# Kernel optimization log

Hardware: AMD Instinct MI355X
Metric: run time of the kernel (lower is better)

The kernel has to match this reference:

```python
import jax, jax.numpy as jnp
import numpy as np

B_, L_, D_, R_, N_ = 8, 1024, 512, 32, 16  # batch, seq(in_channels), dim(=dim_inner), dt_rank, d_state


def setup_inputs() -> dict:
    key = jax.random.key(0)
    ks = jax.random.split(key, 8)
    s = lambda k, shape, scale: jax.random.normal(k, shape, dtype=jnp.float32) * scale
    inv = D_ ** -0.5
    return {
        "x": jax.random.uniform(ks[0], (B_, L_, D_), dtype=jnp.float32),
        "W1": s(ks[1], (D_, D_), inv), "b1": jnp.zeros((D_,), jnp.float32),
        "W2": s(ks[2], (D_, D_), inv), "b2": jnp.zeros((D_,), jnp.float32),
        "Wout": s(ks[3], (D_, D_), inv), "bout": jnp.zeros((D_,), jnp.float32),
        "conv_w": s(ks[4], (L_, L_, 3), (3 * L_) ** -0.5),  # Conv1d(L_, L_, k=3) weight (O,I,W)
        "conv_b": jnp.zeros((L_,), jnp.float32),
        "W_dbc": s(ks[5], (R_ + 2 * N_, D_), inv),          # deltaBC projection (no bias)
        "W_dt": s(ks[6], (D_, R_), R_ ** -0.5),             # dt_proj weight
        "b_dt": jnp.zeros((D_,), jnp.float32),
        "A_log": jnp.log(jnp.tile(jnp.arange(1, N_ + 1, dtype=jnp.float32), (D_, 1))),  # (D, N)
        "Dp": jnp.ones((D_,), jnp.float32),
    }


def _silu(v):
    return v * jax.nn.sigmoid(v)


def _selective_scan(u, delta, A, Bm, Cm, Dp):
    # u, delta: (b, l, d); A: (d, n); Bm, Cm: (b, l, n); Dp: (d,)
    dA = jnp.exp(jnp.einsum('bld,dn->bldn', delta, A))          # (b,l,d,n)
    dBu = jnp.einsum('bld,bln,bld->bldn', delta, Bm, u)          # (b,l,d,n)

    def step(h, inp):
        dA_t, dBu_t, C_t = inp                                   # (b,d,n),(b,d,n),(b,n)
        h = dA_t * h + dBu_t
        return h, jnp.einsum('bdn,bn->bd', h, C_t)

    h0 = jnp.zeros((u.shape[0], u.shape[2], A.shape[1]), u.dtype)
    _, ys = jax.lax.scan(step, h0, (dA.transpose(1, 0, 2, 3), dBu.transpose(1, 0, 2, 3), Cm.transpose(1, 0, 2)))
    return ys.transpose(1, 0, 2) + u * Dp                        # (b,l,d)


def reference(x, W1, b1, W2, b2, Wout, bout, conv_w, conv_b, W_dbc, W_dt, b_dt, A_log, Dp):
    skip = x
    x1 = x @ W1.T + b1                                            # proj_one
    x2 = x @ W2.T + b2                                            # proj_two
    # Conv1d over channel axis = L_ (dim 1), spatial axis = D_ (dim 2)
    x1 = jax.lax.conv_general_dilated(x1, conv_w, window_strides=(1,), padding=((1, 1),),
                                      dimension_numbers=('NCW', 'OIW', 'NCW')) + conv_b[None, :, None]
    x1 = _silu(x1)
    # SSM (zeta-style): deltaBC -> split -> dt_proj -> softplus -> selective scan
    dbc = x1 @ W_dbc.T                                            # (b,l,R+2N)
    delta = jax.nn.softplus(dbc[..., :R_] @ W_dt.T + b_dt)        # (b,l,d)
    Bm, Cm = dbc[..., R_:R_ + N_], dbc[..., R_ + N_:]
    A = -jnp.exp(A_log)
    y = _selective_scan(x1, delta, A, Bm, Cm, Dp)
    out = y * _silu(x2) + skip
    return out @ Wout.T + bout
```

## Files before the change

kernel.cpp:

```cpp
#include <hip/hip_runtime.h>
#include <hip/hip_bf16.h>

typedef __hip_bfloat16 bf16;
typedef __bf16 bf16x8 __attribute__((ext_vector_type(8)));
typedef float f32x4 __attribute__((ext_vector_type(4)));

static_assert(sizeof(bf16) == 2, "bf16 must be 2 bytes");

#define NC 32
#define CH 32
#define X1TP_BSTRIDE (514L * 1024)

__device__ __forceinline__ float silu_f(float v) { return v / (1.0f + __expf(-v)); }

__device__ __forceinline__ void gload16(const bf16* g, bf16* l) {
  __builtin_amdgcn_global_load_lds((const __attribute__((address_space(1))) void*)g,
                                   (__attribute__((address_space(3))) void*)l,
                                   16, 0, 0);
}

template <int N> __device__ __forceinline__ void wait_vm() {
  if constexpr (N == 0)      asm volatile("s_waitcnt vmcnt(0)" ::: "memory");
  else if constexpr (N == 4) asm volatile("s_waitcnt vmcnt(4)" ::: "memory");
  else if constexpr (N == 8) asm volatile("s_waitcnt vmcnt(8)" ::: "memory");
  else static_assert(N == 0 || N == 4 || N == 8, "add case");
}

__global__ __launch_bounds__(256) void prep_all(
    const float* __restrict__ x, const float* __restrict__ W1,
    const float* __restrict__ W2, const float* __restrict__ Wout,
    const float* __restrict__ Wdbc, const float* __restrict__ convw,
    bf16* __restrict__ xb, bf16* __restrict__ w1b, bf16* __restrict__ w2b,
    bf16* __restrict__ woutb, bf16* __restrict__ wdbcb,
    bf16* __restrict__ cws, bf16* __restrict__ x1tp) {
  const int gid = blockIdx.x * 256 + threadIdx.x;
  auto cvt4 = [](const float* src, bf16* dst, long q) {
    float4 v = *reinterpret_cast<const float4*>(src + q * 4);
    ushort4 s;
    s.x = __builtin_bit_cast(unsigned short, __float2bfloat16(v.x));
    s.y = __builtin_bit_cast(unsigned short, __float2bfloat16(v.y));
    s.z = __builtin_bit_cast(unsigned short, __float2bfloat16(v.z));
    s.w = __builtin_bit_cast(unsigned short, __float2bfloat16(v.w));
    *reinterpret_cast<ushort4*>(dst + q * 4) = s;
  };
  if (gid < 1048576) {
    cvt4(x, xb, gid);
  } else if (gid < 1114112) {
    cvt4(W1, w1b, gid - 1048576);
  } else if (gid < 1179648) {
    cvt4(W2, w2b, gid - 1114112);
  } else if (gid < 1245184) {
    cvt4(Wout, woutb, gid - 1179648);
  } else if (gid < 1253376) {
    cvt4(Wdbc, wdbcb, gid - 1245184);
  } else if (gid < 2301952) {
    long idx = gid - 1253376;
    int o = (int)(idx >> 10), i = (int)(idx & 1023);
    float a = convw[idx * 3], b = convw[idx * 3 + 1], c = convw[idx * 3 + 2];
    cws[(long)o * 3072 + i]        = __float2bfloat16(a);
    cws[(long)o * 3072 + 1024 + i] = __float2bfloat16(b);
    cws[(long)o * 3072 + 2048 + i] = __float2bfloat16(c);
  } else {
    int e = gid - 2301952;
    int b = e >> 11, rem = e & 2047;
    int r = rem >> 10, ii = rem & 1023;
    x1tp[(long)b * X1TP_BSTRIDE + (long)r * (513 * 1024) + ii] = __float2bfloat16(0.f);
  }
}

template <int EPI, int BM, int BN, int CONVB>
__device__ __forceinline__ void gemm_body(const bf16* __restrict__ A,
                                          const bf16* __restrict__ Bw,
                                          const float* __restrict__ bias,
                                          float* __restrict__ outf,
                                          bf16* __restrict__ outb,
                                          int M, int N, int K,
                                          long sAz, long sBz, long sOz,
                                          int bx, int by, int z,
                                          bf16* As, bf16* Bs) {
  constexpr int BK = 64;
  constexpr int MI = BM / 32, WNF = BN / 32;
  constexpr int APW = BM / 32, BPW = BN / 32;
  constexpr int IPW = APW + BPW;

  const int tid = threadIdx.x;
  const int w = tid >> 6, l = tid & 63;
  const int wm = w >> 1, wn = w & 1;
  const int m0 = bx * BM, n0 = by * BN;
  const bf16* Ab = A + (long)z * sAz + (long)m0 * K;
  const bf16* Bb = Bw + (long)z * sBz;

  const int lrow = l >> 3;
  const int lcol = (((l & 7) ^ (l >> 3)) << 3);

  auto stage = [&](int buf, int k0) {
#pragma unroll
    for (int j = 0; j < APW; ++j) {
      int iss = w * APW + j;
      int row = iss * 8 + lrow;
      gload16(Ab + (long)row * K + k0 + lcol, &As[buf * BM * 64 + iss * 512]);
    }
#pragma unroll
    for (int j = 0; j < BPW; ++j) {
      int iss = w * BPW + j;
      int row = iss * 8 + lrow;
      const bf16* src;
      if (CONVB) src = Bb + (long)(n0 + row + (k0 >> 10)) * 1024 + (k0 & 1023) + lcol;
      else       src = Bb + (long)(n0 + row) * K + k0 + lcol;
      gload16(src, &Bs[buf * BN * 64 + iss * 512]);
    }
  };

  f32x4 acc[MI][WNF] = {};
  const int nt = K / BK;
  const int lr = l & 15;
  const int lko = (l >> 4) * 8;
  const int xorm = (lr & 7) << 3;

  stage(0, 0);
  for (int t = 0; t < nt; ++t) {
    const int cur = t & 1;
    if (t + 1 < nt) { stage(cur ^ 1, (t + 1) * BK); wait_vm<IPW>(); }
    else            wait_vm<0>();
    __builtin_amdgcn_s_barrier();
    __builtin_amdgcn_sched_barrier(0);
#pragma unroll
    for (int kk = 0; kk < 2; ++kk) {
      const int col = (lko + kk * 32) ^ xorm;
      bf16x8 af[MI], bfg[WNF];
#pragma unroll
      for (int mi = 0; mi < MI; ++mi)
        af[mi] = *reinterpret_cast<const bf16x8*>(
            &As[cur * BM * 64 + (wm * (BM / 2) + mi * 16 + lr) * 64 + col]);
#pragma unroll
      for (int ni = 0; ni < WNF; ++ni)
        bfg[ni] = *reinterpret_cast<const bf16x8*>(
            &Bs[cur * BN * 64 + (wn * (BN / 2) + ni * 16 + lr) * 64 + col]);
#pragma unroll
      for (int mi = 0; mi < MI; ++mi)
#pragma unroll
        for (int ni = 0; ni < WNF; ++ni)
          acc[mi][ni] = __builtin_amdgcn_mfma_f32_16x16x32_bf16(af[mi], bfg[ni], acc[mi][ni], 0, 0, 0);
    }
    __builtin_amdgcn_sched_barrier(0);
    __builtin_amdgcn_s_barrier();
  }

  const int lq = l >> 4;
#pragma unroll
  for (int mi = 0; mi < MI; ++mi) {
#pragma unroll
    for (int ni = 0; ni < WNF; ++ni) {
#pragma unroll
      for (int j = 0; j < 4; ++j) {
        int m = m0 + wm * (BM / 2) + mi * 16 + lq * 4 + j;
        int n = n0 + wn * (BN / 2) + ni * 16 + lr;
        float v = acc[mi][ni][j];
        if (EPI == 2) {
          v += bias[m];
          (outb + (long)z * sOz)[(long)m * N + n] = __float2bfloat16(silu_f(v));
        } else if (EPI == 3) {
          outf[(long)m * N + n] = v;
        } else if (EPI == 4) {
          v += bias[n];
          outf[(long)m * N + n] = v;
        } else if (EPI == 5) {
          v += bias[m];
          int b = n >> 10, li = n & 1023;
          outb[(long)b * X1TP_BSTRIDE + (long)(m + 1) * 1024 + li] = __float2bfloat16(v);
        } else {
          v += bias[n];
          outb[(long)m * N + n] = __float2bfloat16(silu_f(v));
        }
      }
    }
  }
}

template <int EPI, int BM, int BN, int CONVB, int GX, int GY>
__global__ __launch_bounds__(256) void gemm_nt(const bf16* __restrict__ A,
                                               const bf16* __restrict__ Bw,
                                               const float* __restrict__ bias,
                                               float* __restrict__ outf,
                                               bf16* __restrict__ outb,
                                               int M, int N, int K,
                                               long sAz, long sBz, long sOz) {
  __shared__ __align__(16) bf16 As[2 * BM * 64];
  __shared__ __align__(16) bf16 Bs[2 * BN * 64];
  const int bid = (blockIdx.x & 7) * ((int)gridDim.x >> 3) + (blockIdx.x >> 3);
  const int by = bid % GY;
  const int bx = (bid / GY) % GX;
  const int z  = bid / (GX * GY);
  gemm_body<EPI, BM, BN, CONVB>(A, Bw, bias, outf, outb, M, N, K, sAz, sBz, sOz,
                                bx, by, z, As, Bs);
}

__global__ __launch_bounds__(256) void gemm_dual(
    const bf16* __restrict__ w1b, const bf16* __restrict__ xb1,
    const float* __restrict__ b1, bf16* __restrict__ x1tp,
    const bf16* __restrict__ xb2, const bf16* __restrict__ w2b,
    const float* __restrict__ b2, bf16* __restrict__ x2g) {
  __shared__ __align__(16) bf16 As[2 * 128 * 64];
  __shared__ __align__(16) bf16 Bs[2 * 128 * 64];
  int bid = (blockIdx.x & 7) * 64 + (blockIdx.x >> 3);
  if (bid < 256) {
    int by = bid & 63, bx = bid >> 6;
    gemm_body<5, 128, 128, 0>(w1b, xb1, b1, nullptr, x1tp, 512, 8192, 512,
                              0, 0, 0, bx, by, 0, As, Bs);
  } else {
    bid -= 256;
    int by = bid & 3, bx = bid >> 2;
    gemm_body<6, 128, 128, 0>(xb2, w2b, b2, nullptr, x2g, 8192, 512, 512,
                              0, 0, 0, bx, by, 0, As, Bs);
  }
}

__global__ __launch_bounds__(256) void scan_p1(const bf16* __restrict__ u_bf,
                                               const float* __restrict__ dbc,
                                               const float* __restrict__ W_dt,
                                               const float* __restrict__ b_dt,
                                               const float* __restrict__ A_log,
                                               float* __restrict__ P,
                                               float* __restrict__ Q) {
  const int tid = threadIdx.x;
  const int d = blockIdx.x * 256 + tid;
  const int c = blockIdx.y, b = blockIdx.z;
  __shared__ float sD[CH][64];
  for (int i = tid; i < CH * 64; i += 256) {
    int tt = i >> 6, j = i & 63;
    sD[tt][j] = dbc[((long)b * 1024 + c * CH + tt) * 64 + j];
  }
  __syncthreads();
  float wdt[32];
#pragma unroll
  for (int r = 0; r < 32; r += 4) {
    float4 v = *reinterpret_cast<const float4*>(&W_dt[(long)d * 32 + r]);
    wdt[r] = v.x; wdt[r + 1] = v.y; wdt[r + 2] = v.z; wdt[r + 3] = v.w;
  }
  const float bd = b_dt[d];
  float Adn[16];
#pragma unroll
  for (int n = 0; n < 16; ++n) Adn[n] = -__expf(A_log[d * 16 + n]);
  float p[16], q[16];
#pragma unroll
  for (int n = 0; n < 16; ++n) { p[n] = 1.f; q[n] = 0.f; }
  const long rowb = (long)b * 1024 + c * CH;
  for (int tt = 0; tt < CH; ++tt) {
    float a = bd;
#pragma unroll
    for (int r = 0; r < 32; ++r) a = fmaf(sD[tt][r], wdt[r], a);
    float dv = fmaxf(a, 0.f) + log1pf(__expf(-fabsf(a)));
    float uv = __bfloat162float(u_bf[(rowb + tt) * 512 + d]);
    float s = dv * uv;
#pragma unroll
    for (int n = 0; n < 16; ++n) {
      float dA = __expf(dv * Adn[n]);
      p[n] *= dA;
      q[n] = fmaf(dA, q[n], s * sD[tt][32 + n]);
    }
  }
  float* Pp = P + ((long)b * NC + c) * 8192 + (long)d * 16;
  float* Qp = Q + ((long)b * NC + c) * 8192 + (long)d * 16;
#pragma unroll
  for (int n4 = 0; n4 < 4; ++n4) {
    *reinterpret_cast<float4*>(Pp + n4 * 4) = make_float4(p[n4*4], p[n4*4+1], p[n4*4+2], p[n4*4+3]);
    *reinterpret_cast<float4*>(Qp + n4 * 4) = make_float4(q[n4*4], q[n4*4+1], q[n4*4+2], q[n4*4+3]);
  }
}

__global__ __launch_bounds__(256) void scan_p2(const float* __restrict__ P,
                                               const float* __restrict__ Q,
                                               float* __restrict__ Hin) {
  const int dn = blockIdx.x * 256 + threadIdx.x;
  const int b = blockIdx.y;
  float h = 0.f;
#pragma unroll 4
  for (int c = 0; c < NC; ++c) {
    long idx = ((long)b * NC + c) * 8192 + dn;
    Hin[idx] = h;
    h = fmaf(P[idx], h, Q[idx]);
  }
}

__global__ __launch_bounds__(256) void scan_p3(const bf16* __restrict__ u_bf,
                                               const float* __restrict__ dbc,
                                               const float* __restrict__ W_dt,
                                               const float* __restrict__ b_dt,
                                               const float* __restrict__ A_log,
                                               const float* __restrict__ Dp,
                                               const bf16* __restrict__ x2g,
                                               const bf16* __restrict__ xres,
                                               const float* __restrict__ Hin,
                                               bf16* __restrict__ zb) {
  const int tid = threadIdx.x;
  const int d = blockIdx.x * 256 + tid;
  const int c = blockIdx.y, b = blockIdx.z;
  __shared__ float sD[CH][64];
  for (int i = tid; i < CH * 64; i += 256) {
    int tt = i >> 6, j = i & 63;
    sD[tt][j] = dbc[((long)b * 1024 + c * CH + tt) * 64 + j];
  }
  __syncthreads();
  float wdt[32];
#pragma unroll
  for (int r = 0; r < 32; r += 4) {
    float4 v = *reinterpret_cast<const float4*>(&W_dt[(long)d * 32 + r]);
    wdt[r] = v.x; wdt[r + 1] = v.y; wdt[r + 2] = v.z; wdt[r + 3] = v.w;
  }
  const float bd = b_dt[d];
  float Adn[16];
#pragma unroll
  for (int n = 0; n < 16; ++n) Adn[n] = -__expf(A_log[d * 16 + n]);
  float h[16];
  const float* Hp = Hin + ((long)b * NC + c) * 8192 + (long)d * 16;
#pragma unroll
  for (int n4 = 0; n4 < 4; ++n4) {
    float4 v = *reinterpret_cast<const float4*>(Hp + n4 * 4);
    h[n4*4] = v.x; h[n4*4+1] = v.y; h[n4*4+2] = v.z; h[n4*4+3] = v.w;
  }
  const float Dpv = Dp[d];
  const long rowb = (long)b * 1024 + c * CH;
  for (int tt = 0; tt < CH; ++tt) {
    long off = (rowb + tt) * 512 + d;
    float a = bd;
#pragma unroll
    for (int r = 0; r < 32; ++r) a = fmaf(sD[tt][r], wdt[r], a);
    float dv = fmaxf(a, 0.f) + log1pf(__expf(-fabsf(a)));
    float uv = __bfloat162float(u_bf[off]);
    float s = dv * uv;
    float y = uv * Dpv;
#pragma unroll
    for (int n = 0; n < 16; ++n) {
      float dA = __expf(dv * Adn[n]);
      h[n] = fmaf(dA, h[n], s * sD[tt][32 + n]);
      y = fmaf(h[n], sD[tt][48 + n], y);
    }
    float gate = __bfloat162float(x2g[off]);
    float xv = __bfloat162float(xres[off]);
    zb[off] = __float2bfloat16(fmaf(y, gate, xv));
  }
}

extern "C" void kernel_launch(void* const* d_in, const int* in_sizes, int n_in,
                              void* d_out, int out_size, void* d_ws, size_t ws_size,
                              hipStream_t stream) {
  (void)in_sizes; (void)n_in; (void)out_size; (void)ws_size;
  const float* x    = (const float*)d_in[0];
  const float* W1   = (const float*)d_in[1];
  const float* b1   = (const float*)d_in[2];
  const float* W2   = (const float*)d_in[3];
  const float* b2   = (const float*)d_in[4];
  const float* Wout = (const float*)d_in[5];
  const float* bout = (const float*)d_in[6];
  const float* convw = (const float*)d_in[7];
  const float* convb = (const float*)d_in[8];
  const float* Wdbc = (const float*)d_in[9];
  const float* Wdt  = (const float*)d_in[10];
  const float* bdt  = (const float*)d_in[11];
  const float* Alog = (const float*)d_in[12];
  const float* Dp   = (const float*)d_in[13];
  float* out = (float*)d_out;

  char* ws = (char*)d_ws;
  size_t off = 0;
  auto alloc = [&](size_t bytes) { void* p = ws + off; off += (bytes + 255) & ~(size_t)255; return p; };
  bf16* xb     = (bf16*)alloc(8192L * 512 * 2);
  bf16* w1b    = (bf16*)alloc(512L * 512 * 2);
  bf16* w2b    = (bf16*)alloc(512L * 512 * 2);
  bf16* woutb  = (bf16*)alloc(512L * 512 * 2);
  bf16* wdbcb  = (bf16*)alloc(64L * 512 * 2);
  bf16* cws    = (bf16*)alloc(1024L * 3072 * 2);
  bf16* x1tp   = (bf16*)alloc(8L * X1TP_BSTRIDE * 2);
  bf16* x2g    = (bf16*)alloc(8192L * 512 * 2);
  bf16* x1s    = (bf16*)alloc(8192L * 512 * 2);
  float* dbc   = (float*)alloc(8192L * 64 * 4);
  float* P     = (float*)alloc(8L * NC * 8192 * 4);
  float* Q     = (float*)alloc(8L * NC * 8192 * 4);
  float* Hin   = (float*)alloc(8L * NC * 8192 * 4);
  bf16* zb = xb;

  prep_all<<<9056, 256, 0, stream>>>(x, W1, W2, Wout, Wdbc, convw,
                                     xb, w1b, w2b, woutb, wdbcb, cws, x1tp);
  gemm_dual<<<512, 256, 0, stream>>>(w1b, xb, b1, x1tp, xb, w2b, b2, x2g);
  gemm_nt<2, 128, 128, 1, 8, 4><<<256, 256, 0, stream>>>(
      cws, x1tp, convb, nullptr, x1s, 1024, 512, 3072, 0, X1TP_BSTRIDE, 1024L * 512);
  gemm_nt<3, 64, 64, 0, 128, 1><<<128, 256, 0, stream>>>(
      x1s, wdbcb, nullptr, dbc, nullptr, 8192, 64, 512, 0, 0, 0);
  scan_p1<<<dim3(2, NC, 8), 256, 0, stream>>>(x1s, dbc, Wdt, bdt, Alog, P, Q);
  scan_p2<<<dim3(32, 8, 1), 256, 0, stream>>>(P, Q, Hin);
  scan_p3<<<dim3(2, NC, 8), 256, 0, stream>>>(x1s, dbc, Wdt, bdt, Alog, Dp, x2g, xb, Hin, zb);
  gemm_nt<4, 128, 128, 0, 64, 4><<<256, 256, 0, stream>>>(
      zb, woutb, bout, out, nullptr, 8192, 512, 512, 0, 0, 0);
}
```

Before: 179.6 us.

## Fuse scan phases into cooperative kernel, split-K dbc GEMM, triple-buffer GEMMs

The three scan kernels become one cooperative kernel that uses two grid-wide syncs in place of separate launches. The delta/B/C projection GEMM is split four ways along K, and the partial sums are added while loading into shared memory. The conv and output GEMMs move to 64x128 tiles with three-stage buffering and twice as many blocks. This trades launch overhead and low occupancy for grid-sync cost and extra shared memory per block.

```diff
diff --git a/kernel.cpp b/kernel.cpp
--- a/kernel.cpp
+++ b/kernel.cpp
@@ -1,5 +1,8 @@
 #include <hip/hip_runtime.h>
 #include <hip/hip_bf16.h>
+#include <hip/hip_cooperative_groups.h>
+
+namespace cg = cooperative_groups;
 
 typedef __hip_bfloat16 bf16;
 typedef __bf16 bf16x8 __attribute__((ext_vector_type(8)));
@@ -10,6 +13,7 @@
 #define NC 32
 #define CH 32
 #define X1TP_BSTRIDE (514L * 1024)
+#define DBCP (8192L * 64)
 
 __device__ __forceinline__ float silu_f(float v) { return v / (1.0f + __expf(-v)); }
 
@@ -20,10 +24,11 @@
 }
 
 template <int N> __device__ __forceinline__ void wait_vm() {
-  if constexpr (N == 0)      asm volatile("s_waitcnt vmcnt(0)" ::: "memory");
-  else if constexpr (N == 4) asm volatile("s_waitcnt vmcnt(4)" ::: "memory");
-  else if constexpr (N == 8) asm volatile("s_waitcnt vmcnt(8)" ::: "memory");
-  else static_assert(N == 0 || N == 4 || N == 8, "add case");
+  static_assert(N == 0 || N == 4 || N == 8 || N == 12, "add case");
+  if constexpr (N == 0)       asm volatile("s_waitcnt vmcnt(0)" ::: "memory");
+  else if constexpr (N == 4)  asm volatile("s_waitcnt vmcnt(4)" ::: "memory");
+  else if constexpr (N == 8)  asm volatile("s_waitcnt vmcnt(8)" ::: "memory");
+  else if constexpr (N == 12) asm volatile("s_waitcnt vmcnt(12)" ::: "memory");
 }
 
 __global__ __launch_bounds__(256) void prep_all(
@@ -68,13 +73,13 @@
   }
 }
 
-template <int EPI, int BM, int BN, int CONVB>
+template <int EPI, int BM, int BN, int CONVB, int NBUF>
 __device__ __forceinline__ void gemm_body(const bf16* __restrict__ A,
                                           const bf16* __restrict__ Bw,
                                           const float* __restrict__ bias,
                                           float* __restrict__ outf,
                                           bf16* __restrict__ outb,
-                                          int M, int N, int K,
+                                          int M, int N, int K, int lda, int ldb,
                                           long sAz, long sBz, long sOz,
                                           int bx, int by, int z,
                                           bf16* As, bf16* Bs) {
@@ -87,7 +92,7 @@
   const int w = tid >> 6, l = tid & 63;
   const int wm = w >> 1, wn = w & 1;
   const int m0 = bx * BM, n0 = by * BN;
-  const bf16* Ab = A + (long)z * sAz + (long)m0 * K;
+  const bf16* Ab = A + (long)z * sAz + (long)m0 * lda;
   const bf16* Bb = Bw + (long)z * sBz;
 
   const int lrow = l >> 3;
@@ -98,7 +103,7 @@
     for (int j = 0; j < APW; ++j) {
       int iss = w * APW + j;
       int row = iss * 8 + lrow;
-      gload16(Ab + (long)row * K + k0 + lcol, &As[buf * BM * 64 + iss * 512]);
+      gload16(Ab + (long)row * lda + k0 + lcol, &As[buf * BM * 64 + iss * 512]);
     }
 #pragma unroll
     for (int j = 0; j < BPW; ++j) {
@@ -106,7 +111,7 @@
       int row = iss * 8 + lrow;
       const bf16* src;
       if (CONVB) src = Bb + (long)(n0 + row + (k0 >> 10)) * 1024 + (k0 & 1023) + lcol;
-      else       src = Bb + (long)(n0 + row) * K + k0 + lcol;
+      else       src = Bb + (long)(n0 + row) * ldb + k0 + lcol;
       gload16(src, &Bs[buf * BN * 64 + iss * 512]);
     }
   };
@@ -117,11 +122,16 @@
   const int lko = (l >> 4) * 8;
   const int xorm = (lr & 7) << 3;
 
-  stage(0, 0);
+#pragma unroll
+  for (int s = 0; s < NBUF - 1; ++s) stage(s, s * BK);
   for (int t = 0; t < nt; ++t) {
-    const int cur = t & 1;
-    if (t + 1 < nt) { stage(cur ^ 1, (t + 1) * BK); wait_vm<IPW>(); }
-    else            wait_vm<0>();
+    const int cur = t % NBUF;
+    if (t + NBUF - 1 < nt) {
+      stage((t + NBUF - 1) % NBUF, (t + NBUF - 1) * BK);
+      wait_vm<(NBUF - 1) * IPW>();
+    } else {
+      wait_vm<0>();
+    }
     __builtin_amdgcn_s_barrier();
     __builtin_amdgcn_sched_barrier(0);
 #pragma unroll
@@ -160,7 +170,7 @@
           v += bias[m];
           (outb + (long)z * sOz)[(long)m * N + n] = __float2bfloat16(silu_f(v));
         } else if (EPI == 3) {
-          outf[(long)m * N + n] = v;
+          (outf + (long)z * sOz)[(long)m * N + n] = v;
         } else if (EPI == 4) {
           v += bias[n];
           outf[(long)m * N + n] = v;
@@ -177,22 +187,22 @@
   }
 }
 
-template <int EPI, int BM, int BN, int CONVB, int GX, int GY>
+template <int EPI, int BM, int BN, int CONVB, int NBUF, int GX, int GY>
 __global__ __launch_bounds__(256) void gemm_nt(const bf16* __restrict__ A,
                                                const bf16* __restrict__ Bw,
                                                const float* __restrict__ bias,
                                                float* __restrict__ outf,
                                                bf16* __restrict__ outb,
-                                               int M, int N, int K,
+                                               int M, int N, int K, int lda, int ldb,
                                                long sAz, long sBz, long sOz) {
-  __shared__ __align__(16) bf16 As[2 * BM * 64];
-  __shared__ __align__(16) bf16 Bs[2 * BN * 64];
+  __shared__ __align__(16) bf16 As[NBUF * BM * 64];
+  __shared__ __align__(16) bf16 Bs[NBUF * BN * 64];
   const int bid = (blockIdx.x & 7) * ((int)gridDim.x >> 3) + (blockIdx.x >> 3);
   const int by = bid % GY;
   const int bx = (bid / GY) % GX;
   const int z  = bid / (GX * GY);
-  gemm_body<EPI, BM, BN, CONVB>(A, Bw, bias, outf, outb, M, N, K, sAz, sBz, sOz,
-                                bx, by, z, As, Bs);
+  gemm_body<EPI, BM, BN, CONVB, NBUF>(A, Bw, bias, outf, outb, M, N, K, lda, ldb,
+                                      sAz, sBz, sOz, bx, by, z, As, Bs);
 }
 
 __global__ __launch_bounds__(256) void gemm_dual(
@@ -205,30 +215,32 @@
   int bid = (blockIdx.x & 7) * 64 + (blockIdx.x >> 3);
   if (bid < 256) {
     int by = bid & 63, bx = bid >> 6;
-    gemm_body<5, 128, 128, 0>(w1b, xb1, b1, nullptr, x1tp, 512, 8192, 512,
-                              0, 0, 0, bx, by, 0, As, Bs);
+    gemm_body<5, 128, 128, 0, 2>(w1b, xb1, b1, nullptr, x1tp, 512, 8192, 512, 512, 512,
+                                 0, 0, 0, bx, by, 0, As, Bs);
   } else {
     bid -= 256;
     int by = bid & 3, bx = bid >> 2;
-    gemm_body<6, 128, 128, 0>(xb2, w2b, b2, nullptr, x2g, 8192, 512, 512,
-                              0, 0, 0, bx, by, 0, As, Bs);
-  }
-}
-
-__global__ __launch_bounds__(256) void scan_p1(const bf16* __restrict__ u_bf,
-                                               const float* __restrict__ dbc,
-                                               const float* __restrict__ W_dt,
-                                               const float* __restrict__ b_dt,
-                                               const float* __restrict__ A_log,
-                                               float* __restrict__ P,
-                                               float* __restrict__ Q) {
+    gemm_body<6, 128, 128, 0, 2>(xb2, w2b, b2, nullptr, x2g, 8192, 512, 512, 512, 512,
+                                 0, 0, 0, bx, by, 0, As, Bs);
+  }
+}
+
+__global__ __launch_bounds__(256, 2) void scan_fused(
+    const bf16* __restrict__ u_bf, const float* __restrict__ dbc4,
+    const float* __restrict__ W_dt, const float* __restrict__ b_dt,
+    const float* __restrict__ A_log, const float* __restrict__ Dp,
+    const bf16* __restrict__ x2g, const bf16* __restrict__ xres,
+    float* __restrict__ P, float* __restrict__ Q, float* __restrict__ Hin,
+    bf16* __restrict__ zb) {
   const int tid = threadIdx.x;
   const int d = blockIdx.x * 256 + tid;
   const int c = blockIdx.y, b = blockIdx.z;
   __shared__ float sD[CH][64];
   for (int i = tid; i < CH * 64; i += 256) {
     int tt = i >> 6, j = i & 63;
-    sD[tt][j] = dbc[((long)b * 1024 + c * CH + tt) * 64 + j];
+    long base = ((long)b * 1024 + c * CH + tt) * 64 + j;
+    sD[tt][j] = (dbc4[base] + dbc4[base + DBCP]) +
+                (dbc4[base + 2 * DBCP] + dbc4[base + 3 * DBCP]);
   }
   __syncthreads();
   float wdt[32];
@@ -241,103 +253,81 @@
   float Adn[16];
 #pragma unroll
   for (int n = 0; n < 16; ++n) Adn[n] = -__expf(A_log[d * 16 + n]);
-  float p[16], q[16];
-#pragma unroll
-  for (int n = 0; n < 16; ++n) { p[n] = 1.f; q[n] = 0.f; }
   const long rowb = (long)b * 1024 + c * CH;
-  for (int tt = 0; tt < CH; ++tt) {
-    float a = bd;
-#pragma unroll
-    for (int r = 0; r < 32; ++r) a = fmaf(sD[tt][r], wdt[r], a);
-    float dv = fmaxf(a, 0.f) + log1pf(__expf(-fabsf(a)));
-    float uv = __bfloat162float(u_bf[(rowb + tt) * 512 + d]);
-    float s = dv * uv;
-#pragma unroll
-    for (int n = 0; n < 16; ++n) {
-      float dA = __expf(dv * Adn[n]);
-      p[n] *= dA;
-      q[n] = fmaf(dA, q[n], s * sD[tt][32 + n]);
-    }
-  }
-  float* Pp = P + ((long)b * NC + c) * 8192 + (long)d * 16;
-  float* Qp = Q + ((long)b * NC + c) * 8192 + (long)d * 16;
-#pragma unroll
-  for (int n4 = 0; n4 < 4; ++n4) {
-    *reinterpret_cast<float4*>(Pp + n4 * 4) = make_float4(p[n4*4], p[n4*4+1], p[n4*4+2], p[n4*4+3]);
-    *reinterpret_cast<float4*>(Qp + n4 * 4) = make_float4(q[n4*4], q[n4*4+1], q[n4*4+2], q[n4*4+3]);
-  }
-}
-
-__global__ __launch_bounds__(256) void scan_p2(const float* __restrict__ P,
-                                               const float* __restrict__ Q,
-                                               float* __restrict__ Hin) {
-  const int dn = blockIdx.x * 256 + threadIdx.x;
-  const int b = blockIdx.y;
-  float h = 0.f;
-#pragma unroll 4
-  for (int c = 0; c < NC; ++c) {
-    long idx = ((long)b * NC + c) * 8192 + dn;
-    Hin[idx] = h;
-    h = fmaf(P[idx], h, Q[idx]);
-  }
-}
-
-__global__ __launch_bounds__(256) void scan_p3(const bf16* __restrict__ u_bf,
-                                               const float* __restrict__ dbc,
-                                               const float* __restrict__ W_dt,
-                                               const float* __restrict__ b_dt,
-                                               const float* __restrict__ A_log,
-                                               const float* __restrict__ Dp,
-                                               const bf16* __restrict__ x2g,
-                                               const bf16* __restrict__ xres,
-                                               const float* __restrict__ Hin,
-                                               bf16* __restrict__ zb) {
-  const int tid = threadIdx.x;
-  const int d = blockIdx.x * 256 + tid;
-  const int c = blockIdx.y, b = blockIdx.z;
-  __shared__ float sD[CH][64];
-  for (int i = tid; i < CH * 64; i += 256) {
-    int tt = i >> 6, j = i & 63;
-    sD[tt][j] = dbc[((long)b * 1024 + c * CH + tt) * 64 + j];
-  }
-  __syncthreads();
-  float wdt[32];
-#pragma unroll
-  for (int r = 0; r < 32; r += 4) {
-    float4 v = *reinterpret_cast<const float4*>(&W_dt[(long)d * 32 + r]);
-    wdt[r] = v.x; wdt[r + 1] = v.y; wdt[r + 2] = v.z; wdt[r + 3] = v.w;
-  }
-  const float bd = b_dt[d];
-  float Adn[16];
-#pragma unroll
-  for (int n = 0; n < 16; ++n) Adn[n] = -__expf(A_log[d * 16 + n]);
-  float h[16];
-  const float* Hp = Hin + ((long)b * NC + c) * 8192 + (long)d * 16;
-#pragma unroll
-  for (int n4 = 0; n4 < 4; ++n4) {
-    float4 v = *reinterpret_cast<const float4*>(Hp + n4 * 4);
-    h[n4*4] = v.x; h[n4*4+1] = v.y; h[n4*4+2] = v.z; h[n4*4+3] = v.w;
-  }
-  const float Dpv = Dp[d];
-  const long rowb = (long)b * 1024 + c * CH;
-  for (int tt = 0; tt < CH; ++tt) {
-    long off = (rowb + tt) * 512 + d;
-    float a = bd;
-#pragma unroll
-    for (int r = 0; r < 32; ++r) a = fmaf(sD[tt][r], wdt[r], a);
-    float dv = fmaxf(a, 0.f) + log1pf(__expf(-fabsf(a)));
-    float uv = __bfloat162float(u_bf[off]);
-    float s = dv * uv;
-    float y = uv * Dpv;
-#pragma unroll
-    for (int n = 0; n < 16; ++n) {
-      float dA = __expf(dv * Adn[n]);
-      h[n] = fmaf(dA, h[n], s * sD[tt][32 + n]);
-      y = fmaf(h[n], sD[tt][48 + n], y);
-    }
-    float gate = __bfloat162float(x2g[off]);
-    float xv = __bfloat162float(xres[off]);
-    zb[off] = __float2bfloat16(fmaf(y, gate, xv));
+
+  {
+    float p[16], q[16];
+#pragma unroll
+    for (int n = 0; n < 16; ++n) { p[n] = 1.f; q[n] = 0.f; }
+    for (int tt = 0; tt < CH; ++tt) {
+      float a = bd;
+#pragma unroll
+      for (int r = 0; r < 32; ++r) a = fmaf(sD[tt][r], wdt[r], a);
+      float dv = fmaxf(a, 0.f) + log1pf(__expf(-fabsf(a)));
+      float uv = __bfloat162float(u_bf[(rowb + tt) * 512 + d]);
+      float s = dv * uv;
+#pragma unroll
+      for (int n = 0; n < 16; ++n) {
+        float dA = __expf(dv * Adn[n]);
+        p[n] *= dA;
+        q[n] = fmaf(dA, q[n], s * sD[tt][32 + n]);
+      }
+    }
+    float* Pp = P + ((long)b * NC + c) * 8192 + (long)d * 16;
+    float* Qp = Q + ((long)b * NC + c) * 8192 + (long)d * 16;
+#pragma unroll
+    for (int n4 = 0; n4 < 4; ++n4) {
+      *reinterpret_cast<float4*>(Pp + n4 * 4) =
+          make_float4(p[n4 * 4], p[n4 * 4 + 1], p[n4 * 4 + 2], p[n4 * 4 + 3]);
+      *reinterpret_cast<float4*>(Qp + n4 * 4) =
+          make_float4(q[n4 * 4], q[n4 * 4 + 1], q[n4 * 4 + 2], q[n4 * 4 + 3]);
+    }
+  }
+  cg::this_grid().sync();
+
+  {
+    int fb = (blockIdx.z * NC + blockIdx.y) * 2 + blockIdx.x;
+    long gt = (long)fb * 256 + tid;
+    if (gt < 65536) {
+      int bb = (int)(gt >> 13), dn = (int)(gt & 8191);
+      float h = 0.f;
+      for (int c2 = 0; c2 < NC; ++c2) {
+        long idx = ((long)bb * NC + c2) * 8192 + dn;
+        Hin[idx] = h;
+        h = fmaf(P[idx], h, Q[idx]);
+      }
+    }
+  }
+  cg::this_grid().sync();
+
+  {
+    float h[16];
+    const float* Hp = Hin + ((long)b * NC + c) * 8192 + (long)d * 16;
+#pragma unroll
+    for (int n4 = 0; n4 < 4; ++n4) {
+      float4 v = *reinterpret_cast<const float4*>(Hp + n4 * 4);
+      h[n4 * 4] = v.x; h[n4 * 4 + 1] = v.y; h[n4 * 4 + 2] = v.z; h[n4 * 4 + 3] = v.w;
+    }
+    const float Dpv = Dp[d];
+    for (int tt = 0; tt < CH; ++tt) {
+      long off = (rowb + tt) * 512 + d;
+      float a = bd;
+#pragma unroll
+      for (int r = 0; r < 32; ++r) a = fmaf(sD[tt][r], wdt[r], a);
+      float dv = fmaxf(a, 0.f) + log1pf(__expf(-fabsf(a)));
+      float uv = __bfloat162float(u_bf[off]);
+      float s = dv * uv;
+      float y = uv * Dpv;
+#pragma unroll
+      for (int n = 0; n < 16; ++n) {
+        float dA = __expf(dv * Adn[n]);
+        h[n] = fmaf(dA, h[n], s * sD[tt][32 + n]);
+        y = fmaf(h[n], sD[tt][48 + n], y);
+      }
+      float gate = __bfloat162float(x2g[off]);
+      float xv = __bfloat162float(xres[off]);
+      zb[off] = __float2bfloat16(fmaf(y, gate, xv));
+    }
   }
 }
 
@@ -373,7 +363,7 @@
   bf16* x1tp   = (bf16*)alloc(8L * X1TP_BSTRIDE * 2);
   bf16* x2g    = (bf16*)alloc(8192L * 512 * 2);
   bf16* x1s    = (bf16*)alloc(8192L * 512 * 2);
-  float* dbc   = (float*)alloc(8192L * 64 * 4);
+  float* dbc4  = (float*)alloc(4L * DBCP * 4);
   float* P     = (float*)alloc(8L * NC * 8192 * 4);
   float* Q     = (float*)alloc(8L * NC * 8192 * 4);
   float* Hin   = (float*)alloc(8L * NC * 8192 * 4);
@@ -382,13 +372,24 @@
   prep_all<<<9056, 256, 0, stream>>>(x, W1, W2, Wout, Wdbc, convw,
                                      xb, w1b, w2b, woutb, wdbcb, cws, x1tp);
   gemm_dual<<<512, 256, 0, stream>>>(w1b, xb, b1, x1tp, xb, w2b, b2, x2g);
-  gemm_nt<2, 128, 128, 1, 8, 4><<<256, 256, 0, stream>>>(
-      cws, x1tp, convb, nullptr, x1s, 1024, 512, 3072, 0, X1TP_BSTRIDE, 1024L * 512);
-  gemm_nt<3, 64, 64, 0, 128, 1><<<128, 256, 0, stream>>>(
-      x1s, wdbcb, nullptr, dbc, nullptr, 8192, 64, 512, 0, 0, 0);
-  scan_p1<<<dim3(2, NC, 8), 256, 0, stream>>>(x1s, dbc, Wdt, bdt, Alog, P, Q);
-  scan_p2<<<dim3(32, 8, 1), 256, 0, stream>>>(P, Q, Hin);
-  scan_p3<<<dim3(2, NC, 8), 256, 0, stream>>>(x1s, dbc, Wdt, bdt, Alog, Dp, x2g, xb, Hin, zb);
-  gemm_nt<4, 128, 128, 0, 64, 4><<<256, 256, 0, stream>>>(
-      zb, woutb, bout, out, nullptr, 8192, 512, 512, 0, 0, 0);
-}
+  gemm_nt<2, 64, 128, 1, 3, 16, 4><<<512, 256, 0, stream>>>(
+      cws, x1tp, convb, nullptr, x1s, 1024, 512, 3072, 3072, 0,
+      0, X1TP_BSTRIDE, 1024L * 512);
+  gemm_nt<3, 64, 64, 0, 2, 128, 1><<<512, 256, 0, stream>>>(
+      x1s, wdbcb, nullptr, dbc4, nullptr, 8192, 64, 128, 512, 512,
+      128, 128, DBCP);
+  {
+    const bf16* u_arg = x1s;  const float* dbc_arg = dbc4;
+    const float* wdt_arg = Wdt; const float* bdt_arg = bdt;
+    const float* alog_arg = Alog; const float* dp_arg = Dp;
+    const bf16* x2g_arg = x2g; const bf16* xres_arg = xb;
+    float* P_arg = P; float* Q_arg = Q; float* Hin_arg = Hin;
+    bf16* zb_arg = zb;
+    void* sargs[] = {&u_arg, &dbc_arg, &wdt_arg, &bdt_arg, &alog_arg, &dp_arg,
+                     &x2g_arg, &xres_arg, &P_arg, &Q_arg, &Hin_arg, &zb_arg};
+    hipLaunchCooperativeKernel((const void*)scan_fused, dim3(2, NC, 8),
+                               dim3(256, 1, 1), sargs, 0, stream);
+  }
+  gemm_nt<4, 64, 128, 0, 3, 128, 4><<<512, 256, 0, stream>>>(
+      zb, woutb, bout, out, nullptr, 8192, 512, 512, 512, 512, 0, 0, 0);
+}
```

New measurement: 311.9 us. +73.7%, slower.
